# Kernel optimization log

Measured on AMD Instinct MI355X. Metric: run time of the kernel, lower is better.

The kernel has to match this reference:

```python
import jax, jax.numpy as jnp
import numpy as np

B = 2048      # number of enclosing subgraphs
NPG = 100     # nodes per graph (equal-size)
N = B * NPG   # total nodes = 204800
DEG = 8
E = N * DEG   # directed edges = 1638400
HID = 64
NL = 3
MAXZ = 1000
K = 30        # sort-pool k
LAT = HID * NL + 1  # 193 = concat latent dim


def setup_inputs() -> dict:
    key = jax.random.key(0)
    ks = jax.random.split(key, 16)
    rng = np.random.default_rng(0)
    # within-graph random edges: each graph gets E//B edges
    goff = np.repeat(np.arange(B, dtype=np.int64) * NPG, E // B)
    src = rng.integers(0, NPG, size=E) + goff
    dst = rng.integers(0, NPG, size=E) + goff
    edge_index = jnp.asarray(np.stack([src, dst]), dtype=jnp.int32)
    z = jax.random.randint(ks[0], (N,), 0, MAXZ, dtype=jnp.int32)
    batch = (jnp.arange(N, dtype=jnp.int32) // NPG)
    s = 0.1
    d = dict(
        z=z, edge_index=edge_index, batch=batch,
        z_emb=jax.random.normal(ks[1], (MAXZ, HID)) * s,
        W0=jax.random.normal(ks[2], (HID, HID)) * s, b0=jnp.zeros((HID,)),
        W1=jax.random.normal(ks[3], (HID, HID)) * s, b1=jnp.zeros((HID,)),
        W2=jax.random.normal(ks[4], (HID, HID)) * s, b2=jnp.zeros((HID,)),
        W3=jax.random.normal(ks[5], (HID, 1)) * s, b3=jnp.zeros((1,)),
        conv1_w=jax.random.normal(ks[6], (16, 1, LAT)) * s, conv1_b=jnp.zeros((16,)),
        conv2_w=jax.random.normal(ks[7], (32, 16, 5)) * s, conv2_b=jnp.zeros((32,)),
        lin1_w=jax.random.normal(ks[8], (352, 128)) * s, lin1_b=jnp.zeros((128,)),
        lin2_w=jax.random.normal(ks[9], (128, 1)) * s, lin2_b=jnp.zeros((1,)),
    )
    return d


def _conv1d(x, w, stride):
    # x: [B, Cin, L], w: [Cout, Cin, Kw]
    return jax.lax.conv_general_dilated(x, w, window_strides=(stride,),
                                        padding='VALID',
                                        dimension_numbers=('NCH', 'OIH', 'NCH'))


def _gcn(x, W, b, src, dst, dinv):
    # GCNConv with added self-loops and symmetric normalization
    h = x @ W
    norm = dinv[src] * dinv[dst]                      # [E]
    agg = jax.ops.segment_sum(h[src] * norm[:, None], dst, num_segments=N)
    agg = agg + h * (dinv * dinv)[:, None]            # self-loop term
    return agg + b


def reference(z, edge_index, batch, z_emb,
              W0, b0, W1, b1, W2, b2, W3, b3,
              conv1_w, conv1_b, conv2_w, conv2_b,
              lin1_w, lin1_b, lin2_w, lin2_b):
    src, dst = edge_index[0], edge_index[1]
    x = z_emb[z]                                      # [N, HID]
    deg = jnp.zeros((N,), x.dtype).at[dst].add(1.0) + 1.0  # +1 self-loop
    dinv = jax.lax.rsqrt(deg)
    xs = []
    h = x
    for W, b in ((W0, b0), (W1, b1), (W2, b2), (W3, b3)):
        h = jnp.tanh(_gcn(h, W, b, src, dst, dinv))
        xs.append(h)
    x = jnp.concatenate(xs, axis=-1)                  # [N, LAT]
    # global_sort_pool: equal-size graphs -> to_dense_batch is a reshape;
    # sort nodes per graph descending by last channel, keep top-K (NPG>=K)
    xd = x.reshape(B, NPG, LAT)
    order = jnp.argsort(-xd[:, :, -1], axis=1)[:, :K]
    pooled = jnp.take_along_axis(xd, order[:, :, None], axis=1)  # [B,K,LAT]
    v = pooled.reshape(B, 1, K * LAT)
    y = jax.nn.relu(_conv1d(v, conv1_w, LAT) + conv1_b[None, :, None])  # [B,16,30]
    y = y.reshape(B, 16, 15, 2).max(axis=-1)          # MaxPool1d(2,2) -> [B,16,15]
    y = jax.nn.relu(_conv1d(y, conv2_w, 1) + conv2_b[None, :, None])    # [B,32,11]
    y = y.reshape(B, -1)                              # [B,352]
    y = jax.nn.relu(y @ lin1_w + lin1_b)
    # dropout p=0.5 is identity in eval mode
    return y @ lin2_w + lin2_b                        # [B,1]
```

## Files before the change

### kernel.cpp

```cpp
#include <hip/hip_runtime.h>
#include <math.h>

#define NPG  100
#define NGR  2048
#define EPG  800
#define HID  64
#define LATD 193
#define KTOP 30
#define NTHR 1024
#define NWV  16
#define ROWS 7
#define MAXD 32

#define OFF_H64    0
#define OFF_Y1P    0
#define OFF_Y2F    960
#define OFF_PART   2368
#define OFF_O128   6464
#define OFF_Y1     6976
#define OFF_ADJ    51712
#define OFF_Y1ALL  58112
#define OFF_DINV64 64512
#define OFF_KEY64  65320
#define OFF_S4     66120
#define OFF_ZL     66928
#define OFF_SEL    67328
#define OFF_CNT    67456
#define SMEM_SZ    67856

__device__ __forceinline__ double ftanh64(double x) {
    const double y  = fmin(fabs(x) * 2.0, 44.0);
    const double nf = rint(y * 1.4426950408889634074);
    double r = fma(-nf, 6.93147180369123816490e-01, y);
    r = fma(-nf, 1.90821492927058770002e-10, r);
    double p = 2.7557319223985888e-07;
    p = fma(p, r, 2.7557319223985893e-06);
    p = fma(p, r, 2.4801587301587302e-05);
    p = fma(p, r, 1.9841269841269841e-04);
    p = fma(p, r, 1.3888888888888889e-03);
    p = fma(p, r, 8.3333333333333332e-03);
    p = fma(p, r, 4.1666666666666664e-02);
    p = fma(p, r, 1.6666666666666666e-01);
    p = fma(p, r, 0.5);
    p = fma(p, r, 1.0);
    p = fma(p, r, 1.0);
    const double e = p * __longlong_as_double((long long)(1023 + (int)nf) << 52);
    const double d = e + 1.0;
    double rc = (double)(1.0f / (float)d);
    rc = fma(fma(-d, rc, 1.0), rc, rc);
    rc = fma(fma(-d, rc, 1.0), rc, rc);
    const double t = fma(-2.0, rc, 1.0);
    return copysign(t, x);
}

__device__ __forceinline__ void gcnA(
    double* __restrict__ h, const double* __restrict__ dinv,
    const unsigned short* __restrict__ adj, const int* __restrict__ cnt,
    const float* __restrict__ W, const float* __restrict__ b, int lane, int wv)
{
    double acc[ROWS];
#pragma unroll
    for (int i = 0; i < ROWS; ++i) acc[i] = 0.;

#pragma unroll 1
    for (int quarter = 0; quarter < 4; ++quarter) {
        float wf[16];
#pragma unroll
        for (int k = 0; k < 16; ++k) wf[k] = W[(quarter*16 + k)*HID + lane];
#pragma unroll
        for (int i = 0; i < ROWS; ++i) {
            const int n = wv + NWV*i;
            if (n < NPG) {
                const double2* r2 = (const double2*)&h[n*HID + quarter*16];
                double a0=0., a1=0., a2=0., a3=0.;
#pragma unroll
                for (int k2 = 0; k2 < 4; ++k2) {
                    const double2 x01 = r2[2*k2], x23 = r2[2*k2+1];
                    a0 = fma(x01.x, (double)wf[4*k2+0], a0);
                    a1 = fma(x01.y, (double)wf[4*k2+1], a1);
                    a2 = fma(x23.x, (double)wf[4*k2+2], a2);
                    a3 = fma(x23.y, (double)wf[4*k2+3], a3);
                }
                acc[i] += (a0+a1)+(a2+a3);
            }
        }
    }
#pragma unroll
    for (int i = 0; i < ROWS; ++i) {
        const int n = wv + NWV*i;
        if (n < NPG) h[n*HID + lane] = acc[i] * dinv[n];
    }
    __syncthreads();

    const double bj = (double)b[lane];
    const char* hb = (const char*)h + lane*8;
    double agg[ROWS];
#pragma unroll
    for (int i = 0; i < ROWS; ++i) {
        const int n = wv + NWV*i;
        if (n < NPG) {
            const uint4* arow = (const uint4*)&adj[n*MAXD];
            const int dg = cnt[n];
            const int gq = ((dg < MAXD ? dg : MAXD) + 7) >> 3;
            double a0=0., a1=0.;
#pragma unroll 1
            for (int q = 0; q < gq; ++q) {
                const uint4 qq = arow[q];
                a0 += *(const double*)(hb + (qq.x & 0xFFFF));
                a1 += *(const double*)(hb + (qq.x >> 16));
                a0 += *(const double*)(hb + (qq.y & 0xFFFF));
                a1 += *(const double*)(hb + (qq.y >> 16));
                a0 += *(const double*)(hb + (qq.z & 0xFFFF));
                a1 += *(const double*)(hb + (qq.z >> 16));
                a0 += *(const double*)(hb + (qq.w & 0xFFFF));
                a1 += *(const double*)(hb + (qq.w >> 16));
            }
            agg[i] = fma((a0+a1) + h[n*HID+lane], dinv[n], bj);
        }
    }
    __syncthreads();
#pragma unroll
    for (int i = 0; i < ROWS; ++i) {
        const int n = wv + NWV*i;
        if (n < NPG) h[n*HID + lane] = ftanh64(agg[i]);
    }
}

__device__ __forceinline__ void dot_accum(
    const double* __restrict__ h, const float* __restrict__ c1w,
    float* __restrict__ y1all, int lane, int wv, int l)
{
    const int ch = lane >> 2, j = lane & 3;
    const float* wp = &c1w[ch*LATD + l*HID + j*16];
    float wreg[16];
#pragma unroll
    for (int k = 0; k < 16; ++k) wreg[k] = wp[k];
#pragma unroll
    for (int i = 0; i < ROWS; ++i) {
        const int n = wv + NWV*i;
        if (n < NPG) {
            const double* hr = &h[n*HID + j*16];
            float s = 0.f;
#pragma unroll 4
            for (int k = 0; k < 16; ++k) s = fmaf((float)hr[k], wreg[k], s);
            s += __shfl_xor(s, 1, 64);
            s += __shfl_xor(s, 2, 64);
            if (j == 0) y1all[n*16 + ch] += s;
        }
    }
}

__global__ __launch_bounds__(NTHR)
void seal_fused(const int* __restrict__ z,
                const int* __restrict__ esrc, const int* __restrict__ edst,
                const float* __restrict__ zemb,
                const float* __restrict__ W0, const float* __restrict__ b0,
                const float* __restrict__ W1, const float* __restrict__ b1,
                const float* __restrict__ W2, const float* __restrict__ b2,
                const float* __restrict__ W3, const float* __restrict__ b3,
                const float* __restrict__ c1w, const float* __restrict__ c1b,
                const float* __restrict__ c2w, const float* __restrict__ c2b,
                const float* __restrict__ l1w, const float* __restrict__ l1b,
                const float* __restrict__ l2w, const float* __restrict__ l2b,
                float* __restrict__ out)
{
    __shared__ __align__(16) char smem[SMEM_SZ];
    double* h64    = (double*)(smem + OFF_H64);
    unsigned short* adj = (unsigned short*)(smem + OFF_ADJ);
    float*  y1all  = (float*) (smem + OFF_Y1ALL);
    double* dinv64 = (double*)(smem + OFF_DINV64);
    double* key64  = (double*)(smem + OFF_KEY64);
    double* s4     = (double*)(smem + OFF_S4);
    int*    zl     = (int*)   (smem + OFF_ZL);
    int*    sel    = (int*)   (smem + OFF_SEL);
    int*    cnt    = (int*)   (smem + OFF_CNT);
    float*  y1     = (float*) (smem + OFF_Y1);
    float*  y1p    = (float*) (smem + OFF_Y1P);
    float*  y2f    = (float*) (smem + OFF_Y2F);
    float*  part   = (float*) (smem + OFF_PART);
    float*  o128   = (float*) (smem + OFF_O128);

    const int g     = blockIdx.x;
    const int t     = threadIdx.x;
    const int lane  = t & 63;
    const int wv    = t >> 6;
    const int nbase = g * NPG;
    const int ebase = g * EPG;

    int e0s = 0, e0d = -1;
    if (t < EPG) { e0s = esrc[ebase+t] - nbase; e0d = edst[ebase+t] - nbase; }
    for (int i = t; i < NPG; i += NTHR) { zl[i] = z[nbase+i]; cnt[i] = 0; }
    for (int i = t; i < NPG*16; i += NTHR) y1all[i] = 0.f;
    __syncthreads();
    if (e0d >= 0) atomicAdd(&cnt[e0d], 1);
    __syncthreads();
    for (int i = t; i < NPG; i += NTHR) {
        dinv64[i] = 1.0 / sqrt((double)(cnt[i] + 1));
        cnt[i] = 0;
    }
    if (t == 0) s4[NPG] = 0.0;
    __syncthreads();
    if (e0d >= 0) { const int p = atomicAdd(&cnt[e0d], 1); if (p < MAXD) adj[e0d*MAXD + p] = (unsigned short)(e0s << 9); }
    __syncthreads();
    if (t < NPG) {
        const int deg = min(cnt[t], MAXD);
        unsigned short* row = &adj[t*MAXD];
        for (int j = deg; j < MAXD; ++j) row[j] = (unsigned short)(NPG << 9);
        for (int a = 1; a < deg; ++a) {
            const unsigned short x = row[a];
            int bp = a - 1;
            while (bp >= 0 && row[bp] > x) { row[bp+1] = row[bp]; --bp; }
            row[bp+1] = x;
        }
    }
    for (int i = t; i < (NPG+1)*HID; i += NTHR) {
        const int n = i >> 6, k = i & 63;
        h64[i] = (n < NPG) ? (double)zemb[zl[n]*HID + k] : 0.0;
    }
    __syncthreads();

    gcnA(h64, dinv64, adj, cnt, W0, b0, lane, wv);
    dot_accum(h64, c1w, y1all, lane, wv, 0);
    gcnA(h64, dinv64, adj, cnt, W1, b1, lane, wv);
    dot_accum(h64, c1w, y1all, lane, wv, 1);
    gcnA(h64, dinv64, adj, cnt, W2, b2, lane, wv);
    dot_accum(h64, c1w, y1all, lane, wv, 2);

    {
        const float w3f = W3[lane];
        for (int n = wv; n < NPG; n += NWV) {
            double v = h64[n*HID + lane] * (double)w3f;
#pragma unroll
            for (int off = 32; off; off >>= 1) v += __shfl_xor(v, off, 64);
            if (lane == 0) s4[n] = v * dinv64[n];
        }
    }
    __syncthreads();
    if (t < NPG) {
        const char* sb = (const char*)s4;
        const uint4* arow = (const uint4*)&adj[t*MAXD];
        const int dg = min(cnt[t], MAXD);
        const int gq = (dg + 7) >> 3;
        double acc = 0.;
#pragma unroll 1
        for (int q = 0; q < gq; ++q) {
            const uint4 qq = arow[q];
            const double z0 = *(const double*)(sb + ((qq.x & 0xFFFF) >> 6));
            const double z1 = *(const double*)(sb + ((qq.x >> 16)    >> 6));
            const double z2 = *(const double*)(sb + ((qq.y & 0xFFFF) >> 6));
            const double z3 = *(const double*)(sb + ((qq.y >> 16)    >> 6));
            const double z4 = *(const double*)(sb + ((qq.z & 0xFFFF) >> 6));
            const double z5 = *(const double*)(sb + ((qq.z >> 16)    >> 6));
            const double z6 = *(const double*)(sb + ((qq.w & 0xFFFF) >> 6));
            const double z7 = *(const double*)(sb + ((qq.w >> 16)    >> 6));
            acc += ((z0+z1)+(z2+z3)) + ((z4+z5)+(z6+z7));
        }
        key64[t] = ftanh64(fma(acc + s4[t], dinv64[t], (double)b3[0]));
    }
    __syncthreads();
    if (t < NPG) {
        const double kv = key64[t];
        int r = 0;
        for (int m = 0; m < NPG; ++m) {
            const double km = key64[m];
            r += (km > kv) || (km == kv && m < t);
        }
        if (r < KTOP) sel[r] = t;
    }
    __syncthreads();
    if (t < 16*KTOP) {
        const int ch = t & 15, r = t >> 4;
        const int n = sel[r];
        y1[ch*KTOP + r] = y1all[n*16 + ch] + c1b[ch]
                        + (float)key64[n] * c1w[ch*LATD + 192];
    }
    __syncthreads();
    if (t < 16*15) {
        const int ch = t & 15, p = t >> 4;
        y1p[ch*15 + p] = fmaxf(fmaxf(y1[ch*KTOP + 2*p], y1[ch*KTOP + 2*p + 1]), 0.f);
    }
    __syncthreads();
    if (t < 32*11) {
        const int o = t & 31, p = t >> 5;
        float acc = c2b[o];
        const float* wr = &c2w[o*80];
#pragma unroll
        for (int i = 0; i < 16; ++i)
#pragma unroll
            for (int kk = 0; kk < 5; ++kk)
                acc = fmaf(wr[i*5+kk], y1p[i*15 + p + kk], acc);
        y2f[o*11 + p] = fmaxf(acc, 0.f);
    }
    __syncthreads();
    {
        const int j = t & 127, pid = t >> 7;
        const int f0 = pid * 44;
        float acc = 0.f;
        for (int f = f0; f < f0 + 44; ++f) acc = fmaf(y2f[f], l1w[f*128 + j], acc);
        part[pid*128 + j] = acc;
    }
    __syncthreads();
    if (t < 128) {
        float acc = l1b[t];
#pragma unroll
        for (int pid = 0; pid < 8; ++pid) acc += part[pid*128 + t];
        o128[t] = fmaxf(acc, 0.f);
    }
    __syncthreads();
    if (t < 64) {
        float acc = fmaf(o128[t], l2w[t], o128[t+64]*l2w[t+64]);
#pragma unroll
        for (int off = 32; off; off >>= 1) acc += __shfl_xor(acc, off, 64);
        if (t == 0) out[g] = acc + l2b[0];
    }
}

extern "C" void kernel_launch(void* const* d_in, const int* in_sizes, int n_in,
                              void* d_out, int out_size, void* d_ws, size_t ws_size,
                              hipStream_t stream)
{
    const int*   z    = (const int*)d_in[0];
    const int*   ei   = (const int*)d_in[1];
    const float* zemb = (const float*)d_in[3];
    const float* W0   = (const float*)d_in[4];
    const float* b0   = (const float*)d_in[5];
    const float* W1   = (const float*)d_in[6];
    const float* b1   = (const float*)d_in[7];
    const float* W2   = (const float*)d_in[8];
    const float* b2   = (const float*)d_in[9];
    const float* W3   = (const float*)d_in[10];
    const float* b3   = (const float*)d_in[11];
    const float* c1w  = (const float*)d_in[12];
    const float* c1b  = (const float*)d_in[13];
    const float* c2w  = (const float*)d_in[14];
    const float* c2b  = (const float*)d_in[15];
    const float* l1w  = (const float*)d_in[16];
    const float* l1b  = (const float*)d_in[17];
    const float* l2w  = (const float*)d_in[18];
    const float* l2b  = (const float*)d_in[19];
    float*       out  = (float*)d_out;

    const int E = in_sizes[1] / 2;
    seal_fused<<<NGR, NTHR, 0, stream>>>(z, ei, ei + E, zemb,
                                         W0, b0, W1, b1, W2, b2, W3, b3,
                                         c1w, c1b, c2w, c2b, l1w, l1b, l2w, l2b,
                                         out);
}
```

Baseline: 553.4 us.

## Shrink shared memory footprint and embed neighbor group count in adjacency row

Reorganizes shared memory by aliasing zl/cnt onto y1all and moving s4/key64/sel into the overlaid post-GCN region. This cuts LDS usage so more 1024-thread blocks can be resident, and launch bounds are raised to request higher occupancy. The per-node neighbor group count is packed into the low bits of the first adjacency entry, which removes the cnt lookup and peels the first group. dinv is stored as float, which costs a little precision but saves LDS space.

```diff
diff --git a/kernel.cpp b/kernel.cpp
--- a/kernel.cpp
+++ b/kernel.cpp
@@ -13,20 +13,20 @@
 #define MAXD 32
 
 #define OFF_H64    0
+#define OFF_ADJ    51712
+#define OFF_Y1ALL  58112
+#define OFF_DINV   64512
+#define SMEM_SZ    64912
+#define OFF_ZL     OFF_Y1ALL
+#define OFF_CNT    (OFF_Y1ALL + 400)
 #define OFF_Y1P    0
 #define OFF_Y2F    960
 #define OFF_PART   2368
 #define OFF_O128   6464
 #define OFF_Y1     6976
-#define OFF_ADJ    51712
-#define OFF_Y1ALL  58112
-#define OFF_DINV64 64512
-#define OFF_KEY64  65320
-#define OFF_S4     66120
-#define OFF_ZL     66928
-#define OFF_SEL    67328
-#define OFF_CNT    67456
-#define SMEM_SZ    67856
+#define OFF_S4     8896
+#define OFF_KEY64  9704
+#define OFF_SEL    10504
 
 __device__ __forceinline__ double ftanh64(double x) {
     const double y  = fmin(fabs(x) * 2.0, 44.0);
@@ -54,8 +54,8 @@
 }
 
 __device__ __forceinline__ void gcnA(
-    double* __restrict__ h, const double* __restrict__ dinv,
-    const unsigned short* __restrict__ adj, const int* __restrict__ cnt,
+    double* __restrict__ h, const float* __restrict__ dinv,
+    const unsigned short* __restrict__ adj,
     const float* __restrict__ W, const float* __restrict__ b, int lane, int wv)
 {
     double acc[ROWS];
@@ -88,7 +88,7 @@
 #pragma unroll
     for (int i = 0; i < ROWS; ++i) {
         const int n = wv + NWV*i;
-        if (n < NPG) h[n*HID + lane] = acc[i] * dinv[n];
+        if (n < NPG) h[n*HID + lane] = acc[i] * (double)dinv[n];
     }
     __syncthreads();
 
@@ -100,22 +100,30 @@
         const int n = wv + NWV*i;
         if (n < NPG) {
             const uint4* arow = (const uint4*)&adj[n*MAXD];
-            const int dg = cnt[n];
-            const int gq = ((dg < MAXD ? dg : MAXD) + 7) >> 3;
-            double a0=0., a1=0.;
+            const uint4 q0 = arow[0];
+            const int gq = q0.x & 7;
+            double a0, a1;
+            a0  = *(const double*)(hb + (q0.x & 0xFE00));
+            a1  = *(const double*)(hb + (q0.x >> 16));
+            a0 += *(const double*)(hb + (q0.y & 0xFE00));
+            a1 += *(const double*)(hb + (q0.y >> 16));
+            a0 += *(const double*)(hb + (q0.z & 0xFE00));
+            a1 += *(const double*)(hb + (q0.z >> 16));
+            a0 += *(const double*)(hb + (q0.w & 0xFE00));
+            a1 += *(const double*)(hb + (q0.w >> 16));
 #pragma unroll 1
-            for (int q = 0; q < gq; ++q) {
+            for (int q = 1; q < gq; ++q) {
                 const uint4 qq = arow[q];
-                a0 += *(const double*)(hb + (qq.x & 0xFFFF));
+                a0 += *(const double*)(hb + (qq.x & 0xFE00));
                 a1 += *(const double*)(hb + (qq.x >> 16));
-                a0 += *(const double*)(hb + (qq.y & 0xFFFF));
+                a0 += *(const double*)(hb + (qq.y & 0xFE00));
                 a1 += *(const double*)(hb + (qq.y >> 16));
-                a0 += *(const double*)(hb + (qq.z & 0xFFFF));
+                a0 += *(const double*)(hb + (qq.z & 0xFE00));
                 a1 += *(const double*)(hb + (qq.z >> 16));
-                a0 += *(const double*)(hb + (qq.w & 0xFFFF));
+                a0 += *(const double*)(hb + (qq.w & 0xFE00));
                 a1 += *(const double*)(hb + (qq.w >> 16));
             }
-            agg[i] = fma((a0+a1) + h[n*HID+lane], dinv[n], bj);
+            agg[i] = fma((a0+a1) + h[n*HID+lane], (double)dinv[n], bj);
         }
     }
     __syncthreads();
@@ -150,7 +158,7 @@
     }
 }
 
-__global__ __launch_bounds__(NTHR)
+__global__ __launch_bounds__(NTHR, 8)
 void seal_fused(const int* __restrict__ z,
                 const int* __restrict__ esrc, const int* __restrict__ edst,
                 const float* __restrict__ zemb,
@@ -168,12 +176,12 @@
     double* h64    = (double*)(smem + OFF_H64);
     unsigned short* adj = (unsigned short*)(smem + OFF_ADJ);
     float*  y1all  = (float*) (smem + OFF_Y1ALL);
-    double* dinv64 = (double*)(smem + OFF_DINV64);
+    float*  dinv   = (float*) (smem + OFF_DINV);
+    int*    zl     = (int*)   (smem + OFF_ZL);
+    int*    cnt    = (int*)   (smem + OFF_CNT);
+    double* s4     = (double*)(smem + OFF_S4);
     double* key64  = (double*)(smem + OFF_KEY64);
-    double* s4     = (double*)(smem + OFF_S4);
-    int*    zl     = (int*)   (smem + OFF_ZL);
     int*    sel    = (int*)   (smem + OFF_SEL);
-    int*    cnt    = (int*)   (smem + OFF_CNT);
     float*  y1     = (float*) (smem + OFF_Y1);
     float*  y1p    = (float*) (smem + OFF_Y1P);
     float*  y2f    = (float*) (smem + OFF_Y2F);
@@ -190,15 +198,13 @@
     int e0s = 0, e0d = -1;
     if (t < EPG) { e0s = esrc[ebase+t] - nbase; e0d = edst[ebase+t] - nbase; }
     for (int i = t; i < NPG; i += NTHR) { zl[i] = z[nbase+i]; cnt[i] = 0; }
-    for (int i = t; i < NPG*16; i += NTHR) y1all[i] = 0.f;
     __syncthreads();
     if (e0d >= 0) atomicAdd(&cnt[e0d], 1);
     __syncthreads();
     for (int i = t; i < NPG; i += NTHR) {
-        dinv64[i] = 1.0 / sqrt((double)(cnt[i] + 1));
+        dinv[i] = (float)(1.0 / sqrt((double)(cnt[i] + 1)));
         cnt[i] = 0;
     }
-    if (t == 0) s4[NPG] = 0.0;
     __syncthreads();
     if (e0d >= 0) { const int p = atomicAdd(&cnt[e0d], 1); if (p < MAXD) adj[e0d*MAXD + p] = (unsigned short)(e0s << 9); }
     __syncthreads();
@@ -212,50 +218,75 @@
             while (bp >= 0 && row[bp] > x) { row[bp+1] = row[bp]; --bp; }
             row[bp+1] = x;
         }
+        row[0] |= (unsigned short)((deg + 7) >> 3);
     }
     for (int i = t; i < (NPG+1)*HID; i += NTHR) {
         const int n = i >> 6, k = i & 63;
         h64[i] = (n < NPG) ? (double)zemb[zl[n]*HID + k] : 0.0;
     }
     __syncthreads();
-
-    gcnA(h64, dinv64, adj, cnt, W0, b0, lane, wv);
+    for (int i = t; i < NPG*16; i += NTHR) y1all[i] = 0.f;
+
+    gcnA(h64, dinv, adj, W0, b0, lane, wv);
     dot_accum(h64, c1w, y1all, lane, wv, 0);
-    gcnA(h64, dinv64, adj, cnt, W1, b1, lane, wv);
+    gcnA(h64, dinv, adj, W1, b1, lane, wv);
     dot_accum(h64, c1w, y1all, lane, wv, 1);
-    gcnA(h64, dinv64, adj, cnt, W2, b2, lane, wv);
+    gcnA(h64, dinv, adj, W2, b2, lane, wv);
     dot_accum(h64, c1w, y1all, lane, wv, 2);
 
+    double s4r[ROWS];
     {
-        const float w3f = W3[lane];
-        for (int n = wv; n < NPG; n += NWV) {
-            double v = h64[n*HID + lane] * (double)w3f;
-#pragma unroll
-            for (int off = 32; off; off >>= 1) v += __shfl_xor(v, off, 64);
-            if (lane == 0) s4[n] = v * dinv64[n];
-        }
-    }
+        const double w3d = (double)W3[lane];
+#pragma unroll
+        for (int i = 0; i < ROWS; ++i) {
+            const int n = wv + NWV*i;
+            if (n < NPG) {
+                double v = h64[n*HID + lane] * w3d;
+#pragma unroll
+                for (int off = 32; off; off >>= 1) v += __shfl_xor(v, off, 64);
+                s4r[i] = v * (double)dinv[n];
+            }
+        }
+    }
+    __syncthreads();
+#pragma unroll
+    for (int i = 0; i < ROWS; ++i) {
+        const int n = wv + NWV*i;
+        if (n < NPG && lane == 0) s4[n] = s4r[i];
+    }
+    if (t == 0) s4[NPG] = 0.0;
     __syncthreads();
     if (t < NPG) {
         const char* sb = (const char*)s4;
         const uint4* arow = (const uint4*)&adj[t*MAXD];
-        const int dg = min(cnt[t], MAXD);
-        const int gq = (dg + 7) >> 3;
-        double acc = 0.;
+        const uint4 q0 = arow[0];
+        const int gq = q0.x & 7;
+        double acc;
+        {
+            const double z0 = *(const double*)(sb + ((q0.x & 0xFE00) >> 6));
+            const double z1 = *(const double*)(sb + ((q0.x >> 16)    >> 6));
+            const double z2 = *(const double*)(sb + ((q0.y & 0xFE00) >> 6));
+            const double z3 = *(const double*)(sb + ((q0.y >> 16)    >> 6));
+            const double z4 = *(const double*)(sb + ((q0.z & 0xFE00) >> 6));
+            const double z5 = *(const double*)(sb + ((q0.z >> 16)    >> 6));
+            const double z6 = *(const double*)(sb + ((q0.w & 0xFE00) >> 6));
+            const double z7 = *(const double*)(sb + ((q0.w >> 16)    >> 6));
+            acc = ((z0+z1)+(z2+z3)) + ((z4+z5)+(z6+z7));
+        }
 #pragma unroll 1
-        for (int q = 0; q < gq; ++q) {
+        for (int q = 1; q < gq; ++q) {
             const uint4 qq = arow[q];
-            const double z0 = *(const double*)(sb + ((qq.x & 0xFFFF) >> 6));
+            const double z0 = *(const double*)(sb + ((qq.x & 0xFE00) >> 6));
             const double z1 = *(const double*)(sb + ((qq.x >> 16)    >> 6));
-            const double z2 = *(const double*)(sb + ((qq.y & 0xFFFF) >> 6));
+            const double z2 = *(const double*)(sb + ((qq.y & 0xFE00) >> 6));
             const double z3 = *(const double*)(sb + ((qq.y >> 16)    >> 6));
-            const double z4 = *(const double*)(sb + ((qq.z & 0xFFFF) >> 6));
+            const double z4 = *(const double*)(sb + ((qq.z & 0xFE00) >> 6));
             const double z5 = *(const double*)(sb + ((qq.z >> 16)    >> 6));
-            const double z6 = *(const double*)(sb + ((qq.w & 0xFFFF) >> 6));
+            const double z6 = *(const double*)(sb + ((qq.w & 0xFE00) >> 6));
             const double z7 = *(const double*)(sb + ((qq.w >> 16)    >> 6));
             acc += ((z0+z1)+(z2+z3)) + ((z4+z5)+(z6+z7));
         }
-        key64[t] = ftanh64(fma(acc + s4[t], dinv64[t], (double)b3[0]));
+        key64[t] = ftanh64(fma(acc + s4[t], (double)dinv[t], (double)b3[0]));
     }
     __syncthreads();
     if (t < NPG) {
```

Measured after the change: 494.8 us. 1.12x faster.
